# Kernel tuning notes

Measured on AMD Instinct MI355X. Metric: run time of the kernel, lower is better.

Reference implementation:

```python
import jax, jax.numpy as jnp
import numpy as np

N_HEADS = 4
HEAD_DIM = 64
N_EXPERTS = 64
TOP_K = 2
INPUT_DIM = 2048
N_TOKENS = 16384


def setup_inputs() -> dict:
    key = jax.random.key(0)
    ks = jax.random.split(key, 10)
    s = 0.02
    return {
        "x": jax.random.normal(ks[0], (N_TOKENS, INPUT_DIM), dtype=jnp.float32),
        "Wp": jax.random.normal(ks[1], (INPUT_DIM, N_HEADS * HEAD_DIM), dtype=jnp.float32) * s,
        "bp": jnp.zeros((N_HEADS * HEAD_DIM,), dtype=jnp.float32),
        "W1": jax.random.normal(ks[2], (N_HEADS, HEAD_DIM, HEAD_DIM), dtype=jnp.float32) * s,
        "b1": jnp.zeros((N_HEADS, HEAD_DIM), dtype=jnp.float32),
        "W2": jax.random.normal(ks[3], (N_HEADS, HEAD_DIM, N_EXPERTS), dtype=jnp.float32) * s,
        "b2": jnp.zeros((N_HEADS, N_EXPERTS), dtype=jnp.float32),
        "Wc": jax.random.normal(ks[4], (N_HEADS * N_EXPERTS, N_EXPERTS), dtype=jnp.float32) * s,
        "bc": jnp.zeros((N_EXPERTS,), dtype=jnp.float32),
        "temperature": jnp.ones((1,), dtype=jnp.float32) * 2.0,
        "noise_scale": jnp.ones((1,), dtype=jnp.float32) * 0.1,
    }


def reference(x, Wp, bp, W1, b1, W2, b2, Wc, bc, temperature, noise_scale):
    # eval-mode forward (no dropout, no routing noise)
    n = x.shape[0]
    h = (x @ Wp + bp).reshape(n, N_HEADS, HEAD_DIM)            # [N, 4, 64]
    hid = jax.nn.relu(jnp.einsum('nhd,hde->nhe', h, W1) + b1)   # [N, 4, 64]
    head_logits = jnp.einsum('nhd,hde->nhe', hid, W2) + b2      # [N, 4, E] (cat order = head order)
    combined = head_logits.reshape(n, N_HEADS * N_EXPERTS)      # [N, 4*E]
    gate_logits = combined @ Wc + bc                            # [N, E]
    gate_logits = gate_logits / jnp.clip(temperature, 0.5, 5.0)
    top_vals, top_idx = jax.lax.top_k(gate_logits, TOP_K)       # [N, k]
    top_gates = jax.nn.softmax(top_vals, axis=-1)
    gates = jnp.zeros_like(gate_logits).at[jnp.arange(n)[:, None], top_idx].set(top_gates)
    return gates, top_idx, gate_logits
```

## Files before the change

kernel.cpp:

```cpp
#include <hip/hip_runtime.h>
#include <math.h>

#define NT   16384
#define KD   2048
#define PROJ 256
#define NH   4
#define HD   64
#define NE   64

#define GATES_OFF 0
#define IDX_OFF   (NT * NE)
#define GL_OFF    (NT * NE + NT * 2)

typedef __attribute__((ext_vector_type(8))) short short8;
typedef __attribute__((ext_vector_type(4))) float f32x4;

static __device__ __forceinline__ ushort f2bf_rne(float f) {
    uint u = __float_as_uint(f);
    u += 0x7FFFu + ((u >> 16) & 1u);
    return (ushort)(u >> 16);
}
static __device__ __forceinline__ float bf2f(ushort b) {
    return __uint_as_float(((uint)b) << 16);
}

__global__ __launch_bounds__(256) void k0_split(const float* __restrict__ Wp,
                                                ushort* __restrict__ WpT_hi,
                                                ushort* __restrict__ WpT_lo)
{
    const int tid = blockIdx.x * 256 + threadIdx.x;
#pragma unroll
    for (int e = 0; e < 4; ++e) {
        const int idx = tid + e * 131072;
        const int k = idx >> 8, c = idx & 255;
        const float v = Wp[idx];
        const ushort hi = f2bf_rne(v);
        const ushort lo = f2bf_rne(v - bf2f(hi));
        WpT_hi[(size_t)c * KD + k] = hi;
        WpT_lo[(size_t)c * KD + k] = lo;
    }
}

__global__ __launch_bounds__(256) void k1_mfma(const float* __restrict__ x,
                                               const ushort* __restrict__ WpT_hi,
                                               const ushort* __restrict__ WpT_lo,
                                               const float* __restrict__ bp,
                                               float* __restrict__ hT)
{
    __shared__ ushort Ah[2][4096], Al[2][4096];
    __shared__ ushort Bh[2][5120], Bl[2][5120];

    const int t   = threadIdx.x;
    const int wid = t >> 6;
    const int wm  = wid >> 1;
    const int wn  = wid & 1;
    const int l   = t & 63;
    const int m0  = blockIdx.x * 128;
    const int n0  = blockIdx.y * 128;

    f32x4 acc[4][4];
#pragma unroll
    for (int m = 0; m < 4; ++m)
#pragma unroll
        for (int n = 0; n < 4; ++n) acc[m][n] = (f32x4){0.f, 0.f, 0.f, 0.f};

    float4 pa[4];
    uint4  pbh[2], pbl[2];
#pragma unroll
    for (int it = 0; it < 4; ++it) {
        const int fidx = t + it * 256;
        const int arow = fidx >> 3, kq = fidx & 7;
        pa[it] = *(const float4*)&x[(size_t)(m0 + arow) * KD + kq * 4];
    }
#pragma unroll
    for (int it = 0; it < 2; ++it) {
        const int cidx = t + it * 256;
        const int brow = cidx >> 2, q = cidx & 3;
        pbh[it] = *(const uint4*)&WpT_hi[(size_t)(n0 + brow) * KD + q * 8];
        pbl[it] = *(const uint4*)&WpT_lo[(size_t)(n0 + brow) * KD + q * 8];
    }

    const int NTILE = KD / 32;
    for (int ti = 0; ti < NTILE; ++ti) {
        const int buf = ti & 1;
#pragma unroll
        for (int it = 0; it < 4; ++it) {
            const int fidx = t + it * 256;
            const int arow = fidx >> 3, kq = fidx & 7;
            const float vv[4] = { pa[it].x, pa[it].y, pa[it].z, pa[it].w };
            ushort hi[4], lo[4];
#pragma unroll
            for (int e = 0; e < 4; ++e) {
                hi[e] = f2bf_rne(vv[e]);
                lo[e] = f2bf_rne(vv[e] - bf2f(hi[e]));
            }
            const int off = ((arow >> 4) * 64 + (arow & 15) + ((kq >> 1) << 4)) * 8
                          + (kq & 1) * 4;
            uint2 wh = { (uint)hi[0] | ((uint)hi[1] << 16),
                         (uint)hi[2] | ((uint)hi[3] << 16) };
            uint2 wl = { (uint)lo[0] | ((uint)lo[1] << 16),
                         (uint)lo[2] | ((uint)lo[3] << 16) };
            *(uint2*)&Ah[buf][off] = wh;
            *(uint2*)&Al[buf][off] = wl;
        }
#pragma unroll
        for (int it = 0; it < 2; ++it) {
            const int cidx = t + it * 256;
            const int brow = cidx >> 2, q = cidx & 3;
            *(uint4*)&Bh[buf][brow * 40 + q * 8] = pbh[it];
            *(uint4*)&Bl[buf][brow * 40 + q * 8] = pbl[it];
        }
        __syncthreads();
        if (ti + 1 < NTILE) {
            const int kb = (ti + 1) * 32;
#pragma unroll
            for (int it = 0; it < 4; ++it) {
                const int fidx = t + it * 256;
                const int arow = fidx >> 3, kq = fidx & 7;
                pa[it] = *(const float4*)&x[(size_t)(m0 + arow) * KD + kb + kq * 4];
            }
#pragma unroll
            for (int it = 0; it < 2; ++it) {
                const int cidx = t + it * 256;
                const int brow = cidx >> 2, q = cidx & 3;
                pbh[it] = *(const uint4*)&WpT_hi[(size_t)(n0 + brow) * KD + kb + q * 8];
                pbl[it] = *(const uint4*)&WpT_lo[(size_t)(n0 + brow) * KD + kb + q * 8];
            }
        }
        short8 ah[4], al[4], bh[4], bl[4];
#pragma unroll
        for (int m = 0; m < 4; ++m) {
            const int off = ((wm * 4 + m) * 64 + l) * 8;
            ah[m] = *(const short8*)&Ah[buf][off];
            al[m] = *(const short8*)&Al[buf][off];
        }
#pragma unroll
        for (int n = 0; n < 4; ++n) {
            const int row = wn * 64 + n * 16 + (l & 15);
            const int off = row * 40 + (l >> 4) * 8;
            bh[n] = *(const short8*)&Bh[buf][off];
            bl[n] = *(const short8*)&Bl[buf][off];
        }
#pragma unroll
        for (int m = 0; m < 4; ++m)
#pragma unroll
            for (int n = 0; n < 4; ++n) {
                acc[m][n] = __builtin_amdgcn_mfma_f32_16x16x32_bf16(ah[m], bh[n], acc[m][n], 0, 0, 0);
                acc[m][n] = __builtin_amdgcn_mfma_f32_16x16x32_bf16(ah[m], bl[n], acc[m][n], 0, 0, 0);
                acc[m][n] = __builtin_amdgcn_mfma_f32_16x16x32_bf16(al[m], bh[n], acc[m][n], 0, 0, 0);
            }
        __syncthreads();
    }

#pragma unroll
    for (int n = 0; n < 4; ++n) {
        const int col = n0 + wn * 64 + n * 16 + (l & 15);
        const float b = bp[col];
#pragma unroll
        for (int m = 0; m < 4; ++m) {
            const int tok = m0 + wm * 64 + m * 16 + (l >> 4) * 4;
            float4 st = { acc[m][n].x + b, acc[m][n].y + b,
                          acc[m][n].z + b, acc[m][n].w + b };
            *(float4*)&hT[(size_t)col * NT + tok] = st;
        }
    }
}

__global__ __launch_bounds__(256) void k2_heads(const float* __restrict__ hT,
                                                const float* __restrict__ W1,
                                                const float* __restrict__ b1,
                                                const float* __restrict__ W2,
                                                const float* __restrict__ b2,
                                                float* __restrict__ hlT)
{
    __shared__ float W1s[64][64];
    __shared__ float W2s[64][64];
    __shared__ float Hs[64][132];

    const int t    = threadIdx.x;
    const int eg   = t & 15;
    const int tg   = t >> 4;
    const int head = blockIdx.y;
    const int tok0 = blockIdx.x * 128;

    {
        const float4* g1 = (const float4*)(W1 + (size_t)head * HD * HD);
        const float4* g2 = (const float4*)(W2 + (size_t)head * HD * HD);
        float4* s1 = (float4*)&W1s[0][0];
        float4* s2 = (float4*)&W2s[0][0];
#pragma unroll
        for (int q = 0; q < 4; ++q) {
            s1[t + q * 256] = g1[t + q * 256];
            s2[t + q * 256] = g2[t + q * 256];
        }
    }
    const float4 b1v = *(const float4*)&b1[head * HD + eg * 4];
    const float4 b2v = *(const float4*)&b2[head * HD + eg * 4];
    __syncthreads();

    float acc[4][8];
    {
        const float bb[4] = { b1v.x, b1v.y, b1v.z, b1v.w };
#pragma unroll
        for (int j = 0; j < 4; ++j)
#pragma unroll
            for (int i = 0; i < 8; ++i) acc[j][i] = bb[j];
    }
    const float* hbase = &hT[(size_t)(head * HD) * NT + tok0 + tg * 8];
#pragma unroll 4
    for (int d = 0; d < HD; ++d) {
        const float4 w  = *(const float4*)&W1s[d][eg * 4];
        const float4 h0 = *(const float4*)&hbase[(size_t)d * NT];
        const float4 h1 = *(const float4*)&hbase[(size_t)d * NT + 4];
        const float wv[4] = { w.x, w.y, w.z, w.w };
        const float hv[8] = { h0.x, h0.y, h0.z, h0.w, h1.x, h1.y, h1.z, h1.w };
#pragma unroll
        for (int j = 0; j < 4; ++j)
#pragma unroll
            for (int i = 0; i < 8; ++i)
                acc[j][i] = fmaf(wv[j], hv[i], acc[j][i]);
    }
#pragma unroll
    for (int j = 0; j < 4; ++j) {
        float4 lo, hi;
        lo.x = fmaxf(acc[j][0], 0.f); lo.y = fmaxf(acc[j][1], 0.f);
        lo.z = fmaxf(acc[j][2], 0.f); lo.w = fmaxf(acc[j][3], 0.f);
        hi.x = fmaxf(acc[j][4], 0.f); hi.y = fmaxf(acc[j][5], 0.f);
        hi.z = fmaxf(acc[j][6], 0.f); hi.w = fmaxf(acc[j][7], 0.f);
        *(float4*)&Hs[eg * 4 + j][tg * 8]     = lo;
        *(float4*)&Hs[eg * 4 + j][tg * 8 + 4] = hi;
    }
    __syncthreads();

    {
        const float bb[4] = { b2v.x, b2v.y, b2v.z, b2v.w };
#pragma unroll
        for (int j = 0; j < 4; ++j)
#pragma unroll
            for (int i = 0; i < 8; ++i) acc[j][i] = bb[j];
    }
#pragma unroll 4
    for (int d = 0; d < HD; ++d) {
        const float4 w  = *(const float4*)&W2s[d][eg * 4];
        const float4 h0 = *(const float4*)&Hs[d][tg * 8];
        const float4 h1 = *(const float4*)&Hs[d][tg * 8 + 4];
        const float wv[4] = { w.x, w.y, w.z, w.w };
        const float hv[8] = { h0.x, h0.y, h0.z, h0.w, h1.x, h1.y, h1.z, h1.w };
#pragma unroll
        for (int j = 0; j < 4; ++j)
#pragma unroll
            for (int i = 0; i < 8; ++i)
                acc[j][i] = fmaf(wv[j], hv[i], acc[j][i]);
    }
#pragma unroll
    for (int j = 0; j < 4; ++j) {
        float4 lo = { acc[j][0], acc[j][1], acc[j][2], acc[j][3] };
        float4 hi = { acc[j][4], acc[j][5], acc[j][6], acc[j][7] };
        float* dst = &hlT[(size_t)(head * HD + eg * 4 + j) * NT + tok0 + tg * 8];
        *(float4*)&dst[0] = lo;
        *(float4*)&dst[4] = hi;
    }
}

__global__ __launch_bounds__(512) void k3_gate(const float* __restrict__ hlT,
                                               const float* __restrict__ Wc,
                                               const float* __restrict__ bc,
                                               const float* __restrict__ temp,
                                               float* __restrict__ out)
{
    const int t    = threadIdx.x;
    const int eg   = t & 15;
    const int tg   = t >> 4;
    const int tok0 = blockIdx.x * 64;

    const float tv  = fminf(fmaxf(temp[0], 0.5f), 5.0f);
    const float inv = 1.0f / tv;
    const float4 bcv = *(const float4*)&bc[eg * 4];

    float acc[4][2];
    acc[0][0] = bcv.x; acc[0][1] = bcv.x;
    acc[1][0] = bcv.y; acc[1][1] = bcv.y;
    acc[2][0] = bcv.z; acc[2][1] = bcv.z;
    acc[3][0] = bcv.w; acc[3][1] = bcv.w;

    const float* hb = &hlT[tok0 + tg * 2];
#pragma unroll 8
    for (int k = 0; k < PROJ; ++k) {
        const float2 hv = *(const float2*)&hb[(size_t)k * NT];
        const float4 wv = *(const float4*)&Wc[k * NE + eg * 4];
        const float wa[4] = { wv.x, wv.y, wv.z, wv.w };
#pragma unroll
        for (int j = 0; j < 4; ++j) {
            acc[j][0] = fmaf(wa[j], hv.x, acc[j][0]);
            acc[j][1] = fmaf(wa[j], hv.y, acc[j][1]);
        }
    }

#pragma unroll
    for (int i = 0; i < 2; ++i) {
        const int tok = tok0 + tg * 2 + i;
        float gl_[4];
#pragma unroll
        for (int j = 0; j < 4; ++j) gl_[j] = acc[j][i] * inv;

        float v1 = gl_[0]; int i1 = eg * 4;
#pragma unroll
        for (int j = 1; j < 4; ++j)
            if (gl_[j] > v1) { v1 = gl_[j]; i1 = eg * 4 + j; }
#pragma unroll
        for (int off = 8; off >= 1; off >>= 1) {
            const float ov = __shfl_xor(v1, off);
            const int   oi = __shfl_xor(i1, off);
            if (ov > v1 || (ov == v1 && oi < i1)) { v1 = ov; i1 = oi; }
        }
        float v2 = -INFINITY; int i2 = NE;
#pragma unroll
        for (int j = 0; j < 4; ++j) {
            const int e = eg * 4 + j;
            if (e != i1 && gl_[j] > v2) { v2 = gl_[j]; i2 = e; }
        }
#pragma unroll
        for (int off = 8; off >= 1; off >>= 1) {
            const float ov = __shfl_xor(v2, off);
            const int   oi = __shfl_xor(i2, off);
            if (ov > v2 || (ov == v2 && oi < i2)) { v2 = ov; i2 = oi; }
        }

        const float e2  = expf(v2 - v1);
        const float s   = 1.f + e2;
        const float g1v = 1.f / s;
        const float g2v = e2 / s;

        float4 gv;
        {
            const int e0 = eg * 4;
            gv.x = (e0 + 0 == i1) ? g1v : ((e0 + 0 == i2) ? g2v : 0.f);
            gv.y = (e0 + 1 == i1) ? g1v : ((e0 + 1 == i2) ? g2v : 0.f);
            gv.z = (e0 + 2 == i1) ? g1v : ((e0 + 2 == i2) ? g2v : 0.f);
            gv.w = (e0 + 3 == i1) ? g1v : ((e0 + 3 == i2) ? g2v : 0.f);
        }
        *(float4*)&out[GATES_OFF + (size_t)tok * NE + eg * 4] = gv;
        const float4 glv = { gl_[0], gl_[1], gl_[2], gl_[3] };
        *(float4*)&out[GL_OFF + (size_t)tok * NE + eg * 4] = glv;
        if (eg == 0) {
            out[IDX_OFF + (size_t)tok * 2 + 0] = (float)i1;
            out[IDX_OFF + (size_t)tok * 2 + 1] = (float)i2;
        }
    }
}

extern "C" void kernel_launch(void* const* d_in, const int* in_sizes, int n_in,
                              void* d_out, int out_size, void* d_ws, size_t ws_size,
                              hipStream_t stream)
{
    (void)in_sizes; (void)n_in; (void)out_size; (void)ws_size;

    const float* x    = (const float*)d_in[0];
    const float* Wp   = (const float*)d_in[1];
    const float* bp   = (const float*)d_in[2];
    const float* W1   = (const float*)d_in[3];
    const float* b1   = (const float*)d_in[4];
    const float* W2   = (const float*)d_in[5];
    const float* b2   = (const float*)d_in[6];
    const float* Wc   = (const float*)d_in[7];
    const float* bc   = (const float*)d_in[8];
    const float* temp = (const float*)d_in[9];

    float* out = (float*)d_out;
    float* hT  = (float*)d_ws;
    float* hlT = hT + (size_t)PROJ * NT;

    ushort* WpT_hi = (ushort*)hlT;
    ushort* WpT_lo = WpT_hi + (size_t)KD * PROJ;

    k0_split<<<dim3(512),            256, 0, stream>>>(Wp, WpT_hi, WpT_lo);
    k1_mfma <<<dim3(NT / 128, 2),    256, 0, stream>>>(x, WpT_hi, WpT_lo, bp, hT);
    k2_heads<<<dim3(NT / 128, NH),   256, 0, stream>>>(hT, W1, b1, W2, b2, hlT);
    k3_gate <<<dim3(NT / 64),        512, 0, stream>>>(hlT, Wc, bc, temp, out);
}
```

Before: 232.0 us.

## Load Wp fragments straight to registers and unroll k1 pipeline by two

The projection GEMM kernel stops staging the transposed Wp hi/lo tiles through shared memory. Each wave now loads its MFMA B fragments directly from global memory into registers. The K loop is manually unrolled into two ping-pong stages with separate register sets so that loads for the next tile overlap the current MFMAs. The x fp32-to-bf16 hi/lo split now uses truncation instead of round-to-nearest-even, with the residual still captured in the low part, which trims ALU work. The cost is more registers and uncoalesced-ish global reads of B that rely on cache reuse across blocks.

```diff
diff --git a/kernel.cpp b/kernel.cpp
--- a/kernel.cpp
+++ b/kernel.cpp
@@ -48,108 +48,98 @@
                                                float* __restrict__ hT)
 {
     __shared__ ushort Ah[2][4096], Al[2][4096];
-    __shared__ ushort Bh[2][5120], Bl[2][5120];
 
     const int t   = threadIdx.x;
     const int wid = t >> 6;
-    const int wm  = wid >> 1;
+    const int wm4 = (wid >> 1) * 4;
     const int wn  = wid & 1;
     const int l   = t & 63;
     const int m0  = blockIdx.x * 128;
     const int n0  = blockIdx.y * 128;
 
+    const int s0 = t, s1 = t + 256;
+    const float* xa0 = &x[(size_t)(m0 + 16 * (s0 >> 6) + (s0 & 15)) * KD + ((s0 >> 4) & 3) * 8];
+    const float* xa1 = &x[(size_t)(m0 + 16 * (s1 >> 6) + (s1 & 15)) * KD + ((s1 >> 4) & 3) * 8];
+
+    const ushort* wph = &WpT_hi[(size_t)(n0 + wn * 64 + (l & 15)) * KD + (l >> 4) * 8];
+    const ushort* wpl = &WpT_lo[(size_t)(n0 + wn * 64 + (l & 15)) * KD + (l >> 4) * 8];
+
     f32x4 acc[4][4];
 #pragma unroll
     for (int m = 0; m < 4; ++m)
 #pragma unroll
         for (int n = 0; n < 4; ++n) acc[m][n] = (f32x4){0.f, 0.f, 0.f, 0.f};
 
-    float4 pa[4];
-    uint4  pbh[2], pbl[2];
-#pragma unroll
-    for (int it = 0; it < 4; ++it) {
-        const int fidx = t + it * 256;
-        const int arow = fidx >> 3, kq = fidx & 7;
-        pa[it] = *(const float4*)&x[(size_t)(m0 + arow) * KD + kq * 4];
-    }
-#pragma unroll
-    for (int it = 0; it < 2; ++it) {
-        const int cidx = t + it * 256;
-        const int brow = cidx >> 2, q = cidx & 3;
-        pbh[it] = *(const uint4*)&WpT_hi[(size_t)(n0 + brow) * KD + q * 8];
-        pbl[it] = *(const uint4*)&WpT_lo[(size_t)(n0 + brow) * KD + q * 8];
-    }
-
-    const int NTILE = KD / 32;
-    for (int ti = 0; ti < NTILE; ++ti) {
-        const int buf = ti & 1;
-#pragma unroll
-        for (int it = 0; it < 4; ++it) {
-            const int fidx = t + it * 256;
-            const int arow = fidx >> 3, kq = fidx & 7;
-            const float vv[4] = { pa[it].x, pa[it].y, pa[it].z, pa[it].w };
-            ushort hi[4], lo[4];
-#pragma unroll
-            for (int e = 0; e < 4; ++e) {
-                hi[e] = f2bf_rne(vv[e]);
-                lo[e] = f2bf_rne(vv[e] - bf2f(hi[e]));
-            }
-            const int off = ((arow >> 4) * 64 + (arow & 15) + ((kq >> 1) << 4)) * 8
-                          + (kq & 1) * 4;
-            uint2 wh = { (uint)hi[0] | ((uint)hi[1] << 16),
-                         (uint)hi[2] | ((uint)hi[3] << 16) };
-            uint2 wl = { (uint)lo[0] | ((uint)lo[1] << 16),
-                         (uint)lo[2] | ((uint)lo[3] << 16) };
-            *(uint2*)&Ah[buf][off] = wh;
-            *(uint2*)&Al[buf][off] = wl;
-        }
-#pragma unroll
-        for (int it = 0; it < 2; ++it) {
-            const int cidx = t + it * 256;
-            const int brow = cidx >> 2, q = cidx & 3;
-            *(uint4*)&Bh[buf][brow * 40 + q * 8] = pbh[it];
-            *(uint4*)&Bl[buf][brow * 40 + q * 8] = pbl[it];
-        }
+#define K1_STAGE_SLOT(DH, DL, VA, VB)                                          \
+    {                                                                          \
+        const float ff[8] = { (VA).x, (VA).y, (VA).z, (VA).w,                  \
+                              (VB).x, (VB).y, (VB).z, (VB).w };                \
+        uint hp[4], lp[4];                                                     \
+        _Pragma("unroll")                                                      \
+        for (int i = 0; i < 4; ++i) {                                          \
+            const uint u0 = __float_as_uint(ff[2 * i]);                        \
+            const uint u1 = __float_as_uint(ff[2 * i + 1]);                    \
+            hp[i] = (u0 >> 16) | (u1 & 0xFFFF0000u);                           \
+            const float r0 = ff[2 * i]     - __uint_as_float(u0 & 0xFFFF0000u);\
+            const float r1 = ff[2 * i + 1] - __uint_as_float(u1 & 0xFFFF0000u);\
+            lp[i] = (__float_as_uint(r0) >> 16) |                              \
+                    (__float_as_uint(r1) & 0xFFFF0000u);                       \
+        }                                                                      \
+        *(uint4*)(DH) = (uint4){hp[0], hp[1], hp[2], hp[3]};                   \
+        *(uint4*)(DL) = (uint4){lp[0], lp[1], lp[2], lp[3]};                   \
+    }
+
+#define K1_STAGE(BUF, R0, R1, R2, R3)                                          \
+    K1_STAGE_SLOT(&Ah[BUF][s0 * 8], &Al[BUF][s0 * 8], R0, R1);                 \
+    K1_STAGE_SLOT(&Ah[BUF][s1 * 8], &Al[BUF][s1 * 8], R2, R3);
+
+#define K1_LOADA(KB, R0, R1, R2, R3)                                           \
+    R0 = *(const float4*)(xa0 + (KB));                                         \
+    R1 = *(const float4*)(xa0 + (KB) + 4);                                     \
+    R2 = *(const float4*)(xa1 + (KB));                                         \
+    R3 = *(const float4*)(xa1 + (KB) + 4);
+
+#define K1_LOADB(KB, BH, BL)                                                   \
+    _Pragma("unroll")                                                          \
+    for (int n = 0; n < 4; ++n) {                                              \
+        BH[n] = *(const short8*)(wph + (size_t)n * 16 * KD + (KB));            \
+        BL[n] = *(const short8*)(wpl + (size_t)n * 16 * KD + (KB));            \
+    }
+
+#define K1_MFMA(BUF, BH, BL)                                                   \
+    _Pragma("unroll")                                                          \
+    for (int m = 0; m < 4; ++m) {                                              \
+        const short8 ah = *(const short8*)&Ah[BUF][((wm4 + m) * 64 + l) * 8];  \
+        const short8 al = *(const short8*)&Al[BUF][((wm4 + m) * 64 + l) * 8];  \
+        _Pragma("unroll")                                                      \
+        for (int n = 0; n < 4; ++n) {                                          \
+            acc[m][n] = __builtin_amdgcn_mfma_f32_16x16x32_bf16(ah, BH[n], acc[m][n], 0, 0, 0); \
+            acc[m][n] = __builtin_amdgcn_mfma_f32_16x16x32_bf16(ah, BL[n], acc[m][n], 0, 0, 0); \
+            acc[m][n] = __builtin_amdgcn_mfma_f32_16x16x32_bf16(al, BH[n], acc[m][n], 0, 0, 0); \
+        }                                                                      \
+    }
+
+    float4 xA0, xA1, xA2, xA3, xB0, xB1, xB2, xB3;
+    short8 bhA[4], blA[4], bhB[4], blB[4];
+
+    K1_LOADA(0, xA0, xA1, xA2, xA3);
+    K1_LOADB(0, bhA, blA);
+
+    for (int tp = 0; tp < 32; ++tp) {
+        const int kb1 = (2 * tp + 1) * 32;
+        const int kb2 = (2 * tp + 2) * 32;
+        K1_STAGE(0, xA0, xA1, xA2, xA3);
         __syncthreads();
-        if (ti + 1 < NTILE) {
-            const int kb = (ti + 1) * 32;
-#pragma unroll
-            for (int it = 0; it < 4; ++it) {
-                const int fidx = t + it * 256;
-                const int arow = fidx >> 3, kq = fidx & 7;
-                pa[it] = *(const float4*)&x[(size_t)(m0 + arow) * KD + kb + kq * 4];
-            }
-#pragma unroll
-            for (int it = 0; it < 2; ++it) {
-                const int cidx = t + it * 256;
-                const int brow = cidx >> 2, q = cidx & 3;
-                pbh[it] = *(const uint4*)&WpT_hi[(size_t)(n0 + brow) * KD + kb + q * 8];
-                pbl[it] = *(const uint4*)&WpT_lo[(size_t)(n0 + brow) * KD + kb + q * 8];
-            }
-        }
-        short8 ah[4], al[4], bh[4], bl[4];
-#pragma unroll
-        for (int m = 0; m < 4; ++m) {
-            const int off = ((wm * 4 + m) * 64 + l) * 8;
-            ah[m] = *(const short8*)&Ah[buf][off];
-            al[m] = *(const short8*)&Al[buf][off];
-        }
-#pragma unroll
-        for (int n = 0; n < 4; ++n) {
-            const int row = wn * 64 + n * 16 + (l & 15);
-            const int off = row * 40 + (l >> 4) * 8;
-            bh[n] = *(const short8*)&Bh[buf][off];
-            bl[n] = *(const short8*)&Bl[buf][off];
-        }
-#pragma unroll
-        for (int m = 0; m < 4; ++m)
-#pragma unroll
-            for (int n = 0; n < 4; ++n) {
-                acc[m][n] = __builtin_amdgcn_mfma_f32_16x16x32_bf16(ah[m], bh[n], acc[m][n], 0, 0, 0);
-                acc[m][n] = __builtin_amdgcn_mfma_f32_16x16x32_bf16(ah[m], bl[n], acc[m][n], 0, 0, 0);
-                acc[m][n] = __builtin_amdgcn_mfma_f32_16x16x32_bf16(al[m], bh[n], acc[m][n], 0, 0, 0);
-            }
+        K1_LOADA(kb1, xB0, xB1, xB2, xB3);
+        K1_LOADB(kb1, bhB, blB);
+        K1_MFMA(0, bhA, blA);
+        K1_STAGE(1, xB0, xB1, xB2, xB3);
         __syncthreads();
+        if (tp + 1 < 32) {
+            K1_LOADA(kb2, xA0, xA1, xA2, xA3);
+            K1_LOADB(kb2, bhA, blA);
+        }
+        K1_MFMA(1, bhB, blB);
     }
 
 #pragma unroll
@@ -158,12 +148,17 @@
         const float b = bp[col];
 #pragma unroll
         for (int m = 0; m < 4; ++m) {
-            const int tok = m0 + wm * 64 + m * 16 + (l >> 4) * 4;
+            const int tok = m0 + wm4 * 16 + m * 16 + (l >> 4) * 4;
             float4 st = { acc[m][n].x + b, acc[m][n].y + b,
                           acc[m][n].z + b, acc[m][n].w + b };
             *(float4*)&hT[(size_t)col * NT + tok] = st;
         }
     }
+#undef K1_STAGE_SLOT
+#undef K1_STAGE
+#undef K1_LOADA
+#undef K1_LOADB
+#undef K1_MFMA
 }
 
 __global__ __launch_bounds__(256) void k2_heads(const float* __restrict__ hT,
```

Result: no change. 229.7 us (-1.0%).
